# Optimization experiments

Hardware: AMD Instinct MI355X
Metric: run time of the kernel (lower is better)

The kernel has to match this reference:

```python
import jax, jax.numpy as jnp
import numpy as np

N_RAYS = 4096
WORLD_LEN = 160
K0_DIM = 12
WIDTH = 128
VIEWPE = 4
BG_LEN = 0.2
XYZ_MIN = -1.0 - BG_LEN
XYZ_MAX = 1.0 + BG_LEN
ALPHA_INIT = 1e-4
ACT_SHIFT = float(np.log(1.0 / (1.0 - ALPHA_INIT) - 1.0))  # density bias shift
BG = 1.0  # background color (render_kwargs['bg'])
DIM0 = 3 + 3 * VIEWPE * 2 + K0_DIM  # 39


def grid_interp(grid, pts):
    """Trilinear interpolation (align_corners=True). grid: [C,R,R,R], pts: [M,3] world coords -> [M,C]."""
    R = grid.shape[1]
    g = (pts - XYZ_MIN) / (XYZ_MAX - XYZ_MIN) * (R - 1)
    g = jnp.clip(g, 0.0, R - 1)
    g0 = jnp.clip(jnp.floor(g).astype(jnp.int32), 0, R - 2)
    f = g - g0
    x0, y0, z0 = g0[:, 0], g0[:, 1], g0[:, 2]
    fx, fy, fz = f[:, 0], f[:, 1], f[:, 2]

    def gat(i, j, k):
        return grid[:, i, j, k]  # [C, M]

    c00 = gat(x0, y0, z0) * (1 - fz) + gat(x0, y0, z0 + 1) * fz
    c01 = gat(x0, y0 + 1, z0) * (1 - fz) + gat(x0, y0 + 1, z0 + 1) * fz
    c10 = gat(x0 + 1, y0, z0) * (1 - fz) + gat(x0 + 1, y0, z0 + 1) * fz
    c11 = gat(x0 + 1, y0 + 1, z0) * (1 - fz) + gat(x0 + 1, y0 + 1, z0 + 1) * fz
    c0 = c00 * (1 - fy) + c01 * fy
    c1 = c10 * (1 - fy) + c11 * fy
    return (c0 * (1 - fx) + c1 * fx).T  # [M, C]


def setup_inputs() -> dict:
    key = jax.random.key(0)
    ks = jax.random.split(key, 11)
    return {
        "rays_o": jax.random.normal(ks[0], (N_RAYS, 3), jnp.float32) * 0.3,
        "rays_d": jax.random.normal(ks[1], (N_RAYS, 3), jnp.float32),
        "viewdirs": jax.random.normal(ks[2], (N_RAYS, 3), jnp.float32),
        "density_grid": jax.random.normal(ks[3], (1, WORLD_LEN, WORLD_LEN, WORLD_LEN), jnp.float32),
        "k0_grid": jax.random.normal(ks[4], (K0_DIM, WORLD_LEN, WORLD_LEN, WORLD_LEN), jnp.float32),
        "w0": jax.random.normal(ks[5], (DIM0, WIDTH), jnp.float32) * 0.05,
        "b0": jnp.zeros((WIDTH,), jnp.float32),
        "w1": jax.random.normal(ks[6], (WIDTH, WIDTH), jnp.float32) * 0.05,
        "b1": jnp.zeros((WIDTH,), jnp.float32),
        "w2": jax.random.normal(ks[7], (WIDTH, 3), jnp.float32) * 0.05,
        "b2": jnp.zeros((3,), jnp.float32),
        "stepsize": 1,
    }


def reference(rays_o, rays_d, viewdirs, density_grid, k0_grid, w0, b0, w1, b1, w2, b2, stepsize):
    sqrt3 = float(np.sqrt(3.0))
    # --- sample_ray: sample points along rays in the contracted domain ---
    N_inner = int(2.0 / (2.0 + 2.0 * BG_LEN) * sqrt3 * WORLD_LEN / stepsize) + 1
    N_outer = int(N_inner * max(0.01, BG_LEN / 2.0))
    b_inner = jnp.linspace(0.0, 2.0 * sqrt3, N_inner + 1)
    b_outer = 2.0 * sqrt3 / jnp.linspace(1.0, 0.001, N_outer + 1)
    t = jnp.concatenate([(b_inner[1:] + b_inner[:-1]) * 0.5,
                         (b_outer[1:] + b_outer[:-1]) * 0.5])  # [P]
    # scene_center = 0, scene_radius = 1 for xyz_min=-1, xyz_max=1
    rd = rays_d / jnp.linalg.norm(rays_d, axis=-1, keepdims=True)
    pts = rays_o[:, None, :] + rd[:, None, :] * t[None, :, None]  # [N,P,3]
    norm = jnp.max(jnp.abs(pts), axis=-1, keepdims=True)
    safe = jnp.maximum(norm, 1e-9)
    pts = jnp.where(norm <= 1.0, pts, pts / safe * (1.0 + BG_LEN - BG_LEN / safe))
    N, P = pts.shape[0], pts.shape[1]
    flat = pts.reshape(-1, 3)  # [M,3]

    # --- density -> alpha (Raw2Alpha); mask_cache is all-True, fast_color_thres=0 ---
    interval = float(stepsize) * 1.0  # voxel_size_ratio == 1
    dens = grid_interp(density_grid, flat)[:, 0].reshape(N, P)
    alpha = 1.0 - jnp.power(1.0 + jnp.exp(dens + ACT_SHIFT), -interval)

    # --- Alphas2Weights: per-ray alpha compositing ---
    T = jnp.cumprod(1.0 - alpha, axis=1)
    T_excl = jnp.concatenate([jnp.ones((N, 1), T.dtype), T[:, :-1]], axis=1)
    weights = alpha * T_excl  # [N,P]
    alphainv_last = T[:, -1]  # [N]

    # --- k0 features + view-dependent MLP ---
    k0 = grid_interp(k0_grid, flat).reshape(N, P, K0_DIM)
    vf = (2.0 ** jnp.arange(VIEWPE)).astype(rays_o.dtype)
    ve = (viewdirs[..., None] * vf).reshape(N, -1)
    vemb = jnp.concatenate([viewdirs, jnp.sin(ve), jnp.cos(ve)], axis=-1)  # [N, 3+24]
    feat = jnp.concatenate(
        [k0, jnp.broadcast_to(vemb[:, None, :], (N, P, vemb.shape[-1]))], axis=-1)  # [N,P,39]
    h = jax.nn.relu(feat @ w0 + b0)
    h = jax.nn.relu(h @ w1 + b1)
    rgb = jax.nn.sigmoid(h @ w2 + b2)  # [N,P,3]

    # --- volume rendering ---
    rgb_marched = jnp.sum(weights[..., None] * rgb, axis=1) + alphainv_last[:, None] * BG
    return rgb_marched  # [N,3]
```

## Files before the change

kernel.cpp:

```cpp
#include <hip/hip_runtime.h>

#define NRAYS 4096
#define PSAMP 254
#define NIN   231
#define GR    160
#define GR2   25600
#define GR3   4096000
#define SROW  136

typedef __attribute__((ext_vector_type(8))) short bf16x8;
typedef __attribute__((ext_vector_type(4))) float f32x4;

__device__ __forceinline__ unsigned short f2bf(float x) {
    union { float f; unsigned u; } v; v.f = x;
    return (unsigned short)((v.u + 0x7fffu + ((v.u >> 16) & 1u)) >> 16);
}
__device__ __forceinline__ float sigmoidf_(float x) { return 1.0f / (1.0f + __expf(-x)); }

__global__ void prepack(const float* __restrict__ w, unsigned short* __restrict__ out,
                        int K, int N, int ldw, int NT, int KS) {
    const int idx = blockIdx.x * 256 + threadIdx.x;
    if (idx >= NT * KS * 64) return;
    const int l  = idx & 63, f = idx >> 6;
    const int ks = f % KS,  nt = f / KS;
    const int n  = nt * 16 + (l & 15);
    const int k0 = ks * 32 + (l >> 4) * 8;
    unsigned p[4];
    #pragma unroll
    for (int q = 0; q < 4; q++) {
        const int ka = k0 + 2 * q, kb = ka + 1;
        const float va = (ka < K && n < N) ? w[ka * ldw + n] : 0.0f;
        const float vb = (kb < K && n < N) ? w[kb * ldw + n] : 0.0f;
        p[q] = (unsigned)f2bf(va) | ((unsigned)f2bf(vb) << 16);
    }
    uint4 v; v.x = p[0]; v.y = p[1]; v.z = p[2]; v.w = p[3];
    ((uint4*)out)[idx] = v;
}

__global__ __launch_bounds__(256, 2) void voxgo_mfma(
    const float* __restrict__ rays_o, const float* __restrict__ rays_d,
    const float* __restrict__ viewdirs, const float* __restrict__ dg,
    const float* __restrict__ k0g,
    const float* __restrict__ b0, const float* __restrict__ b1,
    const float* __restrict__ b2,
    const unsigned short* __restrict__ pw0, const unsigned short* __restrict__ pw1,
    const unsigned short* __restrict__ pw2,
    float* __restrict__ out)
{
    const int r    = blockIdx.x;
    const int tid  = threadIdx.x;
    const int wv   = tid >> 6, lane = tid & 63, quad = lane >> 4, l16 = lane & 15;

    __shared__ unsigned short hbuf[4][64 * SROW];
    __shared__ float sc[256];
    __shared__ float wgt[256];
    __shared__ float redbuf[256];

    const float ox = rays_o[3*r+0], oy = rays_o[3*r+1], oz = rays_o[3*r+2];
    float dxv = rays_d[3*r+0], dyv = rays_d[3*r+1], dzv = rays_d[3*r+2];
    const float vdx = viewdirs[3*r+0], vdy = viewdirs[3*r+1], vdz = viewdirs[3*r+2];
    const float rinv = rsqrtf(dxv*dxv + dyv*dyv + dzv*dzv);
    dxv *= rinv; dyv *= rinv; dzv *= rinv;

    float t;
    if (tid < NIN) {
        t = ((float)tid + 0.5f) * (2.0f * 1.7320508075688772f / 231.0f);
    } else {
        const float lstep = 0.999f / 23.0f;
        const int j = tid - NIN;
        const float L0 = 1.0f - (float)j * lstep;
        const float L1 = 1.0f - (float)(j+1) * lstep;
        t = 1.7320508075688772f * (1.0f/L0 + 1.0f/L1);
    }

    float px = fmaf(dxv, t, ox), py = fmaf(dyv, t, oy), pz = fmaf(dzv, t, oz);
    const float nrm = fmaxf(fabsf(px), fmaxf(fabsf(py), fabsf(pz)));
    if (nrm > 1.0f) {
        const float s = (1.2f - 0.2f / nrm) / nrm;
        px *= s; py *= s; pz *= s;
    }

    const float gsc = 159.0f / 2.4f;
    const float gx = fminf(fmaxf((px + 1.2f) * gsc, 0.0f), 159.0f);
    const float gy = fminf(fmaxf((py + 1.2f) * gsc, 0.0f), 159.0f);
    const float gz = fminf(fmaxf((pz + 1.2f) * gsc, 0.0f), 159.0f);
    const int x0 = min((int)gx, GR-2), y0 = min((int)gy, GR-2), z0 = min((int)gz, GR-2);
    const float fx = gx - (float)x0, fy = gy - (float)y0, fz = gz - (float)z0;
    const int base = x0*GR2 + y0*GR + z0;

    const float d000 = dg[base],        d001 = dg[base+1];
    const float d010 = dg[base+GR],     d011 = dg[base+GR+1];
    const float d100 = dg[base+GR2],    d101 = dg[base+GR2+1];
    const float d110 = dg[base+GR2+GR], d111 = dg[base+GR2+GR+1];
    const float c00 = d000*(1.0f-fz) + d001*fz;
    const float c01 = d010*(1.0f-fz) + d011*fz;
    const float c10 = d100*(1.0f-fz) + d101*fz;
    const float c11 = d110*(1.0f-fz) + d111*fz;
    const float dens = (c00*(1.0f-fy) + c01*fy)*(1.0f-fx) + (c10*(1.0f-fy) + c11*fy)*fx;

    const float ACT_SHIFT = -9.21024036697535f;
    const float alpha = (tid < PSAMP) ? sigmoidf_(dens + ACT_SHIFT) : 0.0f;

    sc[tid] = 1.0f - alpha;
    __syncthreads();
    #pragma unroll
    for (int off = 1; off < 256; off <<= 1) {
        const float v = (tid >= off) ? sc[tid - off] : 1.0f;
        __syncthreads();
        sc[tid] *= v;
        __syncthreads();
    }
    const float T_excl = (tid == 0) ? 1.0f : sc[tid-1];
    wgt[tid] = alpha * T_excl;

    const float wx0 = 1.0f-fx, wy0 = 1.0f-fy, wz0 = 1.0f-fz;
    const float w000 = wx0*wy0*wz0, w001 = wx0*wy0*fz, w010 = wx0*fy*wz0, w011 = wx0*fy*fz;
    const float w100 = fx*wy0*wz0,  w101 = fx*wy0*fz,  w110 = fx*fy*wz0,  w111 = fx*fy*fz;

    float fv[40];
    #pragma unroll
    for (int c = 0; c < 12; c++) {
        const float* g = k0g + c*GR3 + base;
        fv[c] = w000*g[0]      + w001*g[1]
              + w010*g[GR]     + w011*g[GR+1]
              + w100*g[GR2]    + w101*g[GR2+1]
              + w110*g[GR2+GR] + w111*g[GR2+GR+1];
    }
    fv[12] = vdx; fv[13] = vdy; fv[14] = vdz;
    #pragma unroll
    for (int p = 0; p < 4; p++) {
        const float f = (float)(1 << p);
        fv[15+p] = __sinf(vdx*f);  fv[19+p] = __sinf(vdy*f);  fv[23+p] = __sinf(vdz*f);
        fv[27+p] = __cosf(vdx*f);  fv[31+p] = __cosf(vdy*f);  fv[35+p] = __cosf(vdz*f);
    }
    fv[39] = 0.0f;

    unsigned short* hb = &hbuf[wv][0];
    {
        const int row = tid & 63;
        uint4* dst = (uint4*)(hb + row * SROW);
        #pragma unroll
        for (int i = 0; i < 8; i++) {
            unsigned p[4];
            #pragma unroll
            for (int q = 0; q < 4; q++) {
                const int e0 = i*8 + 2*q, e1 = e0 + 1;
                const unsigned lo = (e0 < 39) ? f2bf(fv[e0]) : 0u;
                const unsigned hi = (e1 < 39) ? f2bf(fv[e1]) : 0u;
                p[q] = lo | (hi << 16);
            }
            uint4 v; v.x = p[0]; v.y = p[1]; v.z = p[2]; v.w = p[3];
            dst[i] = v;
        }
    }
    __syncthreads();


    f32x4 acc1[4][8];
    #pragma unroll
    for (int nt = 0; nt < 8; nt++) {
        const float bz = b0[nt*16 + l16];
        #pragma unroll
        for (int mt = 0; mt < 4; mt++) { f32x4 z = {bz,bz,bz,bz}; acc1[mt][nt] = z; }
    }
    #pragma unroll
    for (int ks = 0; ks < 2; ks++) {
        bf16x8 a[4];
        #pragma unroll
        for (int mt = 0; mt < 4; mt++)
            a[mt] = *(const bf16x8*)(hb + (mt*16 + l16)*SROW + ks*32 + quad*8);
        #pragma unroll
        for (int nt = 0; nt < 8; nt++) {
            const bf16x8 b = *(const bf16x8*)(pw0 + ((nt*2 + ks)*64 + lane)*8);
            #pragma unroll
            for (int mt = 0; mt < 4; mt++)
                acc1[mt][nt] = __builtin_amdgcn_mfma_f32_16x16x32_bf16(a[mt], b, acc1[mt][nt], 0,0,0);
        }
    }
    #pragma unroll
    for (int mt = 0; mt < 4; mt++)
        #pragma unroll
        for (int nt = 0; nt < 8; nt++)
            #pragma unroll
            for (int e = 0; e < 4; e++)
                hb[(mt*16 + quad*4 + e)*SROW + nt*16 + l16] = f2bf(fmaxf(acc1[mt][nt][e], 0.0f));
    __syncthreads();

    f32x4 acc2[4][8];
    #pragma unroll
    for (int nt = 0; nt < 8; nt++) {
        const float bz = b1[nt*16 + l16];
        #pragma unroll
        for (int mt = 0; mt < 4; mt++) { f32x4 z = {bz,bz,bz,bz}; acc2[mt][nt] = z; }
    }
    #pragma unroll
    for (int ks = 0; ks < 4; ks++) {
        bf16x8 a[4];
        #pragma unroll
        for (int mt = 0; mt < 4; mt++)
            a[mt] = *(const bf16x8*)(hb + (mt*16 + l16)*SROW + ks*32 + quad*8);
        #pragma unroll
        for (int nt = 0; nt < 8; nt++) {
            const bf16x8 b = *(const bf16x8*)(pw1 + ((nt*4 + ks)*64 + lane)*8);
            #pragma unroll
            for (int mt = 0; mt < 4; mt++)
                acc2[mt][nt] = __builtin_amdgcn_mfma_f32_16x16x32_bf16(a[mt], b, acc2[mt][nt], 0,0,0);
        }
    }
    #pragma unroll
    for (int mt = 0; mt < 4; mt++)
        #pragma unroll
        for (int nt = 0; nt < 8; nt++)
            #pragma unroll
            for (int e = 0; e < 4; e++)
                hb[(mt*16 + quad*4 + e)*SROW + nt*16 + l16] = f2bf(fmaxf(acc2[mt][nt][e], 0.0f));
    __syncthreads();

    f32x4 acc3[4];
    {
        const float bz = (l16 < 3) ? b2[l16] : 0.0f;
        #pragma unroll
        for (int mt = 0; mt < 4; mt++) { f32x4 z = {bz,bz,bz,bz}; acc3[mt] = z; }
    }
    #pragma unroll
    for (int ks = 0; ks < 4; ks++) {
        const bf16x8 b = *(const bf16x8*)(pw2 + (ks*64 + lane)*8);
        #pragma unroll
        for (int mt = 0; mt < 4; mt++) {
            const bf16x8 a = *(const bf16x8*)(hb + (mt*16 + l16)*SROW + ks*32 + quad*8);
            acc3[mt] = __builtin_amdgcn_mfma_f32_16x16x32_bf16(a, b, acc3[mt], 0,0,0);
        }
    }

    float contrib = 0.0f;
    #pragma unroll
    for (int mt = 0; mt < 4; mt++)
        #pragma unroll
        for (int e = 0; e < 4; e++) {
            const float s = sigmoidf_(acc3[mt][e]);
            contrib += wgt[wv*64 + mt*16 + quad*4 + e] * s;
        }
    redbuf[tid] = contrib;
    __syncthreads();
    if (tid < 3) {
        float acc_o = sc[PSAMP-1];
        #pragma unroll
        for (int w = 0; w < 4; w++)
            #pragma unroll
            for (int q = 0; q < 4; q++)
                acc_o += redbuf[w*64 + q*16 + tid];
        out[3*r + tid] = acc_o;
    }
}

extern "C" void kernel_launch(void* const* d_in, const int* in_sizes, int n_in,
                              void* d_out, int out_size, void* d_ws, size_t ws_size,
                              hipStream_t stream) {
    (void)in_sizes; (void)n_in; (void)out_size; (void)ws_size;
    unsigned short* pw0 = (unsigned short*)d_ws;
    unsigned short* pw1 = pw0 + 16*64*8;
    unsigned short* pw2 = pw1 + 32*64*8;

    prepack<<<4, 256, 0, stream>>>((const float*)d_in[5], pw0,  39, 128, 128, 8, 2);
    prepack<<<8, 256, 0, stream>>>((const float*)d_in[7], pw1, 128, 128, 128, 8, 4);
    prepack<<<1, 256, 0, stream>>>((const float*)d_in[9], pw2, 128,   3,   3, 1, 4);

    voxgo_mfma<<<NRAYS, 256, 0, stream>>>(
        (const float*)d_in[0],
        (const float*)d_in[1],
        (const float*)d_in[2],
        (const float*)d_in[3],
        (const float*)d_in[4],
        (const float*)d_in[6],
        (const float*)d_in[8],
        (const float*)d_in[10],
        pw0, pw1, pw2,
        (float*)d_out);
}
```

Measured before the change: 524.0 us.

## Repack density and k0 grids into interleaved fp16 voxel records for gather

Adds a pre-pass that converts the 12-channel k0 grid and the density grid into one fp16 record of 16 halves (32 bytes) per voxel. The main kernel then fetches each trilinear corner with two 16-byte loads instead of 13 scattered fp32 loads from separate channel planes. The cost is a full-grid repack each call, which reads about 200MB and writes about 130MB, plus fp16 rounding of the grid values. The path runs only when the workspace is large enough, otherwise it falls back to the old fp32 kernel.

```diff
diff --git a/kernel.cpp b/kernel.cpp
--- a/kernel.cpp
+++ b/kernel.cpp
@@ -16,6 +16,20 @@
     return (unsigned short)((v.u + 0x7fffu + ((v.u >> 16) & 1u)) >> 16);
 }
 __device__ __forceinline__ float sigmoidf_(float x) { return 1.0f / (1.0f + __expf(-x)); }
+
+__device__ __forceinline__ unsigned packh2(float a, float b) {
+    union { _Float16 h; unsigned short u; } ua, ub;
+    ua.h = (_Float16)a; ub.h = (_Float16)b;
+    return (unsigned)ua.u | ((unsigned)ub.u << 16);
+}
+__device__ __forceinline__ float h2f(unsigned u16) {
+    union { unsigned short u; _Float16 h; } v; v.u = (unsigned short)u16;
+    return (float)v.h;
+}
+__device__ __forceinline__ float cget(const uint4& q, int c) {
+    const unsigned w = ((const unsigned*)&q)[c >> 1];
+    return h2f((c & 1) ? (w >> 16) : (w & 0xffffu));
+}
 
 __global__ void prepack(const float* __restrict__ w, unsigned short* __restrict__ out,
                         int K, int N, int ldw, int NT, int KS) {
@@ -37,7 +51,268 @@
     ((uint4*)out)[idx] = v;
 }
 
-__global__ __launch_bounds__(256, 2) void voxgo_mfma(
+__global__ __launch_bounds__(256) void repack_grid(
+    const float* __restrict__ dg, const float* __restrict__ k0g,
+    unsigned short* __restrict__ pg)
+{
+    const int i2 = blockIdx.x * 256 + threadIdx.x;
+    if (i2 >= GR3 / 2) return;
+    unsigned ow[16];
+    #pragma unroll
+    for (int c = 0; c < 12; c += 2) {
+        const float2 va = ((const float2*)(k0g + (size_t)c       * GR3))[i2];
+        const float2 vb = ((const float2*)(k0g + (size_t)(c + 1) * GR3))[i2];
+        ow[(c >> 1)]     = packh2(va.x, vb.x);
+        ow[8 + (c >> 1)] = packh2(va.y, vb.y);
+    }
+    const float2 dv = ((const float2*)dg)[i2];
+    ow[6]  = packh2(dv.x, 0.0f);
+    ow[14] = packh2(dv.y, 0.0f);
+    ow[7] = 0u; ow[15] = 0u;
+    uint4* dst = (uint4*)(pg + (size_t)i2 * 32);
+    dst[0] = make_uint4(ow[0],  ow[1],  ow[2],  ow[3]);
+    dst[1] = make_uint4(ow[4],  ow[5],  ow[6],  ow[7]);
+    dst[2] = make_uint4(ow[8],  ow[9],  ow[10], ow[11]);
+    dst[3] = make_uint4(ow[12], ow[13], ow[14], ow[15]);
+}
+
+__global__ __launch_bounds__(256, 2) void voxgo_mfma_pk(
+    const float* __restrict__ rays_o, const float* __restrict__ rays_d,
+    const float* __restrict__ viewdirs,
+    const unsigned short* __restrict__ pg,
+    const float* __restrict__ b0, const float* __restrict__ b1,
+    const float* __restrict__ b2,
+    const unsigned short* __restrict__ pw0, const unsigned short* __restrict__ pw1,
+    const unsigned short* __restrict__ pw2,
+    float* __restrict__ out)
+{
+    const int r    = blockIdx.x;
+    const int tid  = threadIdx.x;
+    const int wv   = tid >> 6, lane = tid & 63, quad = lane >> 4, l16 = lane & 15;
+
+    __shared__ unsigned short hbuf[4][64 * SROW];
+    __shared__ float sc[256];
+    __shared__ float wgt[256];
+    __shared__ float redbuf[256];
+
+    const float ox = rays_o[3*r+0], oy = rays_o[3*r+1], oz = rays_o[3*r+2];
+    float dxv = rays_d[3*r+0], dyv = rays_d[3*r+1], dzv = rays_d[3*r+2];
+    const float vdx = viewdirs[3*r+0], vdy = viewdirs[3*r+1], vdz = viewdirs[3*r+2];
+    const float rinv = rsqrtf(dxv*dxv + dyv*dyv + dzv*dzv);
+    dxv *= rinv; dyv *= rinv; dzv *= rinv;
+
+    float t;
+    if (tid < NIN) {
+        t = ((float)tid + 0.5f) * (2.0f * 1.7320508075688772f / 231.0f);
+    } else {
+        const float lstep = 0.999f / 23.0f;
+        const int j = tid - NIN;
+        const float L0 = 1.0f - (float)j * lstep;
+        const float L1 = 1.0f - (float)(j+1) * lstep;
+        t = 1.7320508075688772f * (1.0f/L0 + 1.0f/L1);
+    }
+
+    float px = fmaf(dxv, t, ox), py = fmaf(dyv, t, oy), pz = fmaf(dzv, t, oz);
+    const float nrm = fmaxf(fabsf(px), fmaxf(fabsf(py), fabsf(pz)));
+    if (nrm > 1.0f) {
+        const float s = (1.2f - 0.2f / nrm) / nrm;
+        px *= s; py *= s; pz *= s;
+    }
+
+    const float gsc = 159.0f / 2.4f;
+    const float gx = fminf(fmaxf((px + 1.2f) * gsc, 0.0f), 159.0f);
+    const float gy = fminf(fmaxf((py + 1.2f) * gsc, 0.0f), 159.0f);
+    const float gz = fminf(fmaxf((pz + 1.2f) * gsc, 0.0f), 159.0f);
+    const int x0 = min((int)gx, GR-2), y0 = min((int)gy, GR-2), z0 = min((int)gz, GR-2);
+    const float fx = gx - (float)x0, fy = gy - (float)y0, fz = gz - (float)z0;
+    const int base = x0*GR2 + y0*GR + z0;
+
+    const unsigned short* cp = pg + (size_t)base * 16;
+    uint4 hi[8], lo[8];
+    #pragma unroll
+    for (int j = 0; j < 8; j++) {
+        const int off = ((j >> 2) * GR2 + ((j >> 1) & 1) * GR + (j & 1)) * 16;
+        hi[j] = *((const uint4*)(cp + off) + 1);
+    }
+    #pragma unroll
+    for (int j = 0; j < 8; j++) {
+        const int off = ((j >> 2) * GR2 + ((j >> 1) & 1) * GR + (j & 1)) * 16;
+        lo[j] = *((const uint4*)(cp + off));
+    }
+
+    float fv[40];
+    fv[12] = vdx; fv[13] = vdy; fv[14] = vdz;
+    #pragma unroll
+    for (int p = 0; p < 4; p++) {
+        const float f = (float)(1 << p);
+        fv[15+p] = __sinf(vdx*f);  fv[19+p] = __sinf(vdy*f);  fv[23+p] = __sinf(vdz*f);
+        fv[27+p] = __cosf(vdx*f);  fv[31+p] = __cosf(vdy*f);  fv[35+p] = __cosf(vdz*f);
+    }
+    fv[39] = 0.0f;
+
+    float dcr[8];
+    #pragma unroll
+    for (int j = 0; j < 8; j++) dcr[j] = h2f(hi[j].z & 0xffffu);
+    const float c00 = dcr[0]*(1.0f-fz) + dcr[1]*fz;
+    const float c01 = dcr[2]*(1.0f-fz) + dcr[3]*fz;
+    const float c10 = dcr[4]*(1.0f-fz) + dcr[5]*fz;
+    const float c11 = dcr[6]*(1.0f-fz) + dcr[7]*fz;
+    const float dens = (c00*(1.0f-fy) + c01*fy)*(1.0f-fx) + (c10*(1.0f-fy) + c11*fy)*fx;
+
+    const float ACT_SHIFT = -9.21024036697535f;
+    const float alpha = (tid < PSAMP) ? sigmoidf_(dens + ACT_SHIFT) : 0.0f;
+
+    sc[tid] = 1.0f - alpha;
+    __syncthreads();
+    #pragma unroll
+    for (int off = 1; off < 256; off <<= 1) {
+        const float v = (tid >= off) ? sc[tid - off] : 1.0f;
+        __syncthreads();
+        sc[tid] *= v;
+        __syncthreads();
+    }
+    const float T_excl = (tid == 0) ? 1.0f : sc[tid-1];
+    wgt[tid] = alpha * T_excl;
+
+    const float wx0 = 1.0f-fx, wy0 = 1.0f-fy, wz0 = 1.0f-fz;
+    const float w000 = wx0*wy0*wz0, w001 = wx0*wy0*fz, w010 = wx0*fy*wz0, w011 = wx0*fy*fz;
+    const float w100 = fx*wy0*wz0,  w101 = fx*wy0*fz,  w110 = fx*fy*wz0,  w111 = fx*fy*fz;
+
+    #pragma unroll
+    for (int c = 0; c < 12; c++) {
+        float s;
+        if (c < 8) {
+            s = w000*cget(lo[0],c) + w001*cget(lo[1],c)
+              + w010*cget(lo[2],c) + w011*cget(lo[3],c)
+              + w100*cget(lo[4],c) + w101*cget(lo[5],c)
+              + w110*cget(lo[6],c) + w111*cget(lo[7],c);
+        } else {
+            s = w000*cget(hi[0],c-8) + w001*cget(hi[1],c-8)
+              + w010*cget(hi[2],c-8) + w011*cget(hi[3],c-8)
+              + w100*cget(hi[4],c-8) + w101*cget(hi[5],c-8)
+              + w110*cget(hi[6],c-8) + w111*cget(hi[7],c-8);
+        }
+        fv[c] = s;
+    }
+
+    unsigned short* hb = &hbuf[wv][0];
+    {
+        const int row = tid & 63;
+        uint4* dst = (uint4*)(hb + row * SROW);
+        #pragma unroll
+        for (int i = 0; i < 8; i++) {
+            unsigned p[4];
+            #pragma unroll
+            for (int q = 0; q < 4; q++) {
+                const int e0 = i*8 + 2*q, e1 = e0 + 1;
+                const unsigned plo = (e0 < 39) ? f2bf(fv[e0]) : 0u;
+                const unsigned phi = (e1 < 39) ? f2bf(fv[e1]) : 0u;
+                p[q] = plo | (phi << 16);
+            }
+            uint4 v; v.x = p[0]; v.y = p[1]; v.z = p[2]; v.w = p[3];
+            dst[i] = v;
+        }
+    }
+    __syncthreads();
+
+    f32x4 acc1[4][8];
+    #pragma unroll
+    for (int nt = 0; nt < 8; nt++) {
+        const float bz = b0[nt*16 + l16];
+        #pragma unroll
+        for (int mt = 0; mt < 4; mt++) { f32x4 z = {bz,bz,bz,bz}; acc1[mt][nt] = z; }
+    }
+    #pragma unroll
+    for (int ks = 0; ks < 2; ks++) {
+        bf16x8 a[4];
+        #pragma unroll
+        for (int mt = 0; mt < 4; mt++)
+            a[mt] = *(const bf16x8*)(hb + (mt*16 + l16)*SROW + ks*32 + quad*8);
+        #pragma unroll
+        for (int nt = 0; nt < 8; nt++) {
+            const bf16x8 b = *(const bf16x8*)(pw0 + ((nt*2 + ks)*64 + lane)*8);
+            #pragma unroll
+            for (int mt = 0; mt < 4; mt++)
+                acc1[mt][nt] = __builtin_amdgcn_mfma_f32_16x16x32_bf16(a[mt], b, acc1[mt][nt], 0,0,0);
+        }
+    }
+    #pragma unroll
+    for (int mt = 0; mt < 4; mt++)
+        #pragma unroll
+        for (int nt = 0; nt < 8; nt++)
+            #pragma unroll
+            for (int e = 0; e < 4; e++)
+                hb[(mt*16 + quad*4 + e)*SROW + nt*16 + l16] = f2bf(fmaxf(acc1[mt][nt][e], 0.0f));
+    __syncthreads();
+
+    f32x4 acc2[4][8];
+    #pragma unroll
+    for (int nt = 0; nt < 8; nt++) {
+        const float bz = b1[nt*16 + l16];
+        #pragma unroll
+        for (int mt = 0; mt < 4; mt++) { f32x4 z = {bz,bz,bz,bz}; acc2[mt][nt] = z; }
+    }
+    #pragma unroll
+    for (int ks = 0; ks < 4; ks++) {
+        bf16x8 a[4];
+        #pragma unroll
+        for (int mt = 0; mt < 4; mt++)
+            a[mt] = *(const bf16x8*)(hb + (mt*16 + l16)*SROW + ks*32 + quad*8);
+        #pragma unroll
+        for (int nt = 0; nt < 8; nt++) {
+            const bf16x8 b = *(const bf16x8*)(pw1 + ((nt*4 + ks)*64 + lane)*8);
+            #pragma unroll
+            for (int mt = 0; mt < 4; mt++)
+                acc2[mt][nt] = __builtin_amdgcn_mfma_f32_16x16x32_bf16(a[mt], b, acc2[mt][nt], 0,0,0);
+        }
+    }
+    #pragma unroll
+    for (int mt = 0; mt < 4; mt++)
+        #pragma unroll
+        for (int nt = 0; nt < 8; nt++)
+            #pragma unroll
+            for (int e = 0; e < 4; e++)
+                hb[(mt*16 + quad*4 + e)*SROW + nt*16 + l16] = f2bf(fmaxf(acc2[mt][nt][e], 0.0f));
+    __syncthreads();
+
+    f32x4 acc3[4];
+    {
+        const float bz = (l16 < 3) ? b2[l16] : 0.0f;
+        #pragma unroll
+        for (int mt = 0; mt < 4; mt++) { f32x4 z = {bz,bz,bz,bz}; acc3[mt] = z; }
+    }
+    #pragma unroll
+    for (int ks = 0; ks < 4; ks++) {
+        const bf16x8 b = *(const bf16x8*)(pw2 + (ks*64 + lane)*8);
+        #pragma unroll
+        for (int mt = 0; mt < 4; mt++) {
+            const bf16x8 a = *(const bf16x8*)(hb + (mt*16 + l16)*SROW + ks*32 + quad*8);
+            acc3[mt] = __builtin_amdgcn_mfma_f32_16x16x32_bf16(a, b, acc3[mt], 0,0,0);
+        }
+    }
+
+    float contrib = 0.0f;
+    #pragma unroll
+    for (int mt = 0; mt < 4; mt++)
+        #pragma unroll
+        for (int e = 0; e < 4; e++) {
+            const float s = sigmoidf_(acc3[mt][e]);
+            contrib += wgt[wv*64 + mt*16 + quad*4 + e] * s;
+        }
+    redbuf[tid] = contrib;
+    __syncthreads();
+    if (tid < 3) {
+        float acc_o = sc[PSAMP-1];
+        #pragma unroll
+        for (int w = 0; w < 4; w++)
+            #pragma unroll
+            for (int q = 0; q < 4; q++)
+                acc_o += redbuf[w*64 + q*16 + tid];
+        out[3*r + tid] = acc_o;
+    }
+}
+
+__global__ __launch_bounds__(256, 2) void voxgo_mfma_f32(
     const float* __restrict__ rays_o, const float* __restrict__ rays_d,
     const float* __restrict__ viewdirs, const float* __restrict__ dg,
     const float* __restrict__ k0g,
@@ -145,9 +420,9 @@
             #pragma unroll
             for (int q = 0; q < 4; q++) {
                 const int e0 = i*8 + 2*q, e1 = e0 + 1;
-                const unsigned lo = (e0 < 39) ? f2bf(fv[e0]) : 0u;
-                const unsigned hi = (e1 < 39) ? f2bf(fv[e1]) : 0u;
-                p[q] = lo | (hi << 16);
+                const unsigned lov = (e0 < 39) ? f2bf(fv[e0]) : 0u;
+                const unsigned hiv = (e1 < 39) ? f2bf(fv[e1]) : 0u;
+                p[q] = lov | (hiv << 16);
             }
             uint4 v; v.x = p[0]; v.y = p[1]; v.z = p[2]; v.w = p[3];
             dst[i] = v;
@@ -155,7 +430,6 @@
     }
     __syncthreads();
 
-
     f32x4 acc1[4][8];
     #pragma unroll
     for (int nt = 0; nt < 8; nt++) {
@@ -256,24 +530,42 @@
 extern "C" void kernel_launch(void* const* d_in, const int* in_sizes, int n_in,
                               void* d_out, int out_size, void* d_ws, size_t ws_size,
                               hipStream_t stream) {
-    (void)in_sizes; (void)n_in; (void)out_size; (void)ws_size;
-    unsigned short* pw0 = (unsigned short*)d_ws;
-    unsigned short* pw1 = pw0 + 16*64*8;
-    unsigned short* pw2 = pw1 + 32*64*8;
-
-    prepack<<<4, 256, 0, stream>>>((const float*)d_in[5], pw0,  39, 128, 128, 8, 2);
-    prepack<<<8, 256, 0, stream>>>((const float*)d_in[7], pw1, 128, 128, 128, 8, 4);
-    prepack<<<1, 256, 0, stream>>>((const float*)d_in[9], pw2, 128,   3,   3, 1, 4);
-
-    voxgo_mfma<<<NRAYS, 256, 0, stream>>>(
-        (const float*)d_in[0],
-        (const float*)d_in[1],
-        (const float*)d_in[2],
-        (const float*)d_in[3],
-        (const float*)d_in[4],
-        (const float*)d_in[6],
-        (const float*)d_in[8],
-        (const float*)d_in[10],
-        pw0, pw1, pw2,
-        (float*)d_out);
-}
+    (void)in_sizes; (void)n_in; (void)out_size;
+    const size_t PG_BYTES = (size_t)GR3 * 32;
+    const size_t PW_BYTES = (size_t)(16 + 32 + 4) * 64 * 8 * 2;
+
+    if (ws_size >= PG_BYTES + PW_BYTES) {
+        unsigned short* pg  = (unsigned short*)d_ws;
+        unsigned short* pw0 = (unsigned short*)((char*)d_ws + PG_BYTES);
+        unsigned short* pw1 = pw0 + 16*64*8;
+        unsigned short* pw2 = pw1 + 32*64*8;
+
+        repack_grid<<<GR3/512, 256, 0, stream>>>(
+            (const float*)d_in[3], (const float*)d_in[4], pg);
+        prepack<<<4, 256, 0, stream>>>((const float*)d_in[5], pw0,  39, 128, 128, 8, 2);
+        prepack<<<8, 256, 0, stream>>>((const float*)d_in[7], pw1, 128, 128, 128, 8, 4);
+        prepack<<<1, 256, 0, stream>>>((const float*)d_in[9], pw2, 128,   3,   3, 1, 4);
+
+        voxgo_mfma_pk<<<NRAYS, 256, 0, stream>>>(
+            (const float*)d_in[0], (const float*)d_in[1], (const float*)d_in[2],
+            pg,
+            (const float*)d_in[6], (const float*)d_in[8], (const float*)d_in[10],
+            pw0, pw1, pw2,
+            (float*)d_out);
+    } else {
+        unsigned short* pw0 = (unsigned short*)d_ws;
+        unsigned short* pw1 = pw0 + 16*64*8;
+        unsigned short* pw2 = pw1 + 32*64*8;
+
+        prepack<<<4, 256, 0, stream>>>((const float*)d_in[5], pw0,  39, 128, 128, 8, 2);
+        prepack<<<8, 256, 0, stream>>>((const float*)d_in[7], pw1, 128, 128, 128, 8, 4);
+        prepack<<<1, 256, 0, stream>>>((const float*)d_in[9], pw2, 128,   3,   3, 1, 4);
+
+        voxgo_mfma_f32<<<NRAYS, 256, 0, stream>>>(
+            (const float*)d_in[0], (const float*)d_in[1], (const float*)d_in[2],
+            (const float*)d_in[3], (const float*)d_in[4],
+            (const float*)d_in[6], (const float*)d_in[8], (const float*)d_in[10],
+            pw0, pw1, pw2,
+            (float*)d_out);
+    }
+}
```

Result: faster. 457.4 us (-12.7%).
